# Performance work log

Hardware: AMD Instinct MI355X
Metric: run time of the kernel (lower is better)

## Reference

```python
import math
import jax, jax.numpy as jnp
import numpy as np

B, T, D, H = 2, 2048, 768, 12
DH = D // H
EPS = 1e-5


def setup_inputs() -> dict:
    key = jax.random.key(0)
    ks = jax.random.split(key, 8)
    s = 0.02
    x = jax.random.normal(ks[0], (B, T, D), dtype=jnp.float32)
    lengths = jax.random.randint(ks[1], (B,), T // 2, T + 1)
    lengths = lengths.at[0].set(T)  # ensure max(lengths)==T (static shape)
    return {
        'x': x,
        'lengths': lengths,
        'w_qkv': jax.random.normal(ks[2], (D, 3 * D), dtype=jnp.float32) * s,
        'b_qkv': jnp.zeros((3 * D,), jnp.float32),
        'w_proj': jax.random.normal(ks[3], (D, D), dtype=jnp.float32) * s,
        'b_proj': jnp.zeros((D,), jnp.float32),
        'ln1_g': jnp.ones((D,), jnp.float32),
        'ln1_b': jnp.zeros((D,), jnp.float32),
        'w_fc': jax.random.normal(ks[4], (D, 4 * D), dtype=jnp.float32) * s,
        'b_fc': jnp.zeros((4 * D,), jnp.float32),
        'w_out': jax.random.normal(ks[5], (4 * D, D), dtype=jnp.float32) * s,
        'b_out': jnp.zeros((D,), jnp.float32),
        'ln2_g': jnp.ones((D,), jnp.float32),
        'ln2_b': jnp.zeros((D,), jnp.float32),
    }


def _gelu(x):
    c = math.sqrt(2.0 / math.pi)
    return 0.5 * x * (1.0 + jnp.tanh(c * (x + 0.044715 * x * x * x)))


def _layernorm(x, g, b):
    mu = jnp.mean(x, axis=-1, keepdims=True)
    var = jnp.mean(jnp.square(x - mu), axis=-1, keepdims=True)
    return (x - mu) * jax.lax.rsqrt(var + EPS) * g + b


def _block(x, lengths, w_qkv, b_qkv, w_proj, b_proj, ln1_g, ln1_b,
           w_fc, b_fc, w_out, b_out, ln2_g, ln2_b):
    dt = x.dtype
    # [B, T] validity mask from ragged lengths
    pos = jnp.arange(T)
    mask = (pos[None, :] < lengths[:, None]).astype(dt)

    # --- SeqMultiHeadAttention (scale=False) ---
    qkv = x @ w_qkv + b_qkv  # [B, T, 3D]
    q, k, v = jnp.split(qkv, 3, axis=-1)

    def split_heads(t):  # [B,T,D] -> [B,H,T,DH]
        return t.reshape(B, T, H, DH).transpose(0, 2, 1, 3)

    q, k, v = split_heads(q), split_heads(k), split_heads(v)
    w = jnp.einsum('bhqd,bhkd->bhqk', q, k)  # [B,H,T,T]
    amask = (mask[:, None, :, None] * mask[:, None, None, :])  # [B,1,T,T]
    w = w * amask + (-1e9) * (1.0 - amask)
    w = jax.nn.softmax(w, axis=-1) * amask
    a = jnp.einsum('bhqk,bhkd->bhqd', w, v)  # [B,H,T,DH]
    a = a.transpose(0, 2, 1, 3).reshape(B, T, D)
    a = a @ w_proj + b_proj

    # --- SeqLayerNorm 1: pack/unpack == per-position LN, padding zeroed ---
    n = _layernorm(x + a, ln1_g, ln1_b) * mask[..., None]

    # --- MLP (gelu) ---
    m = _gelu(n @ w_fc + b_fc) @ w_out + b_out

    # --- SeqLayerNorm 2 ---
    h = _layernorm(n + m, ln2_g, ln2_b) * mask[..., None]
    return h


def reference(x, lengths, w_qkv, b_qkv, w_proj, b_proj, ln1_g, ln1_b,
              w_fc, b_fc, w_out, b_out, ln2_g, ln2_b):
    return _block(x, lengths, w_qkv, b_qkv, w_proj, b_proj, ln1_g, ln1_b,
                  w_fc, b_fc, w_out, b_out, ln2_g, ln2_b)
```

## Files before the change

kernel.cpp:

```cpp
#include <hip/hip_runtime.h>
#include <hip/hip_bf16.h>
#include <math.h>

constexpr int Bc  = 2;
constexpr int Tc  = 2048;
constexpr int Dc  = 768;
constexpr int Hc  = 12;
constexpr int DHc = 64;
constexpr int M_ROWS = Bc * Tc;
constexpr int D3  = 3 * Dc;
constexpr int D4  = 4 * Dc;

typedef __attribute__((ext_vector_type(8))) short short8;
typedef __attribute__((ext_vector_type(4))) float f32x4;

__device__ __forceinline__ unsigned short f2bf(float v) {
    union { __hip_bfloat16 b; unsigned short u; } cv;
    cv.b = __float2bfloat16(v);
    return cv.u;
}
__device__ __forceinline__ float bf2f(unsigned short u) {
    union { __hip_bfloat16 b; unsigned short u; } cv;
    cv.u = u;
    return __bfloat162float(cv.b);
}
__device__ __forceinline__ void bsplit(float v, unsigned short& h, unsigned short& l) {
    h = f2bf(v);
    l = f2bf(v - bf2f(h));
}

__device__ __forceinline__ float gelu_f(float x) {
    const float c = 0.79788456080286535588f;
    return 0.5f * x * (1.0f + tanhf(c * (x + 0.044715f * x * x * x)));
}

__device__ __forceinline__ void glds16(const unsigned short* g, unsigned short* l) {
    __builtin_amdgcn_global_load_lds(
        (const __attribute__((address_space(1))) void*)g,
        (__attribute__((address_space(3))) void*)l, 16, 0, 0);
}

__device__ __forceinline__ void tcast8(
    const float* __restrict__ w, int ldw,
    unsigned short* __restrict__ th, int K, int N, int idx)
{
    const int n  = idx % N;
    const int k0 = (idx / N) * 8;
    unsigned short hv[8];
#pragma unroll
    for (int j = 0; j < 8; ++j)
        hv[j] = f2bf(w[(size_t)(k0 + j) * ldw + n]);
    const size_t o = (size_t)n * K + k0;
    *(ushort4*)(th + o)     = make_ushort4(hv[0], hv[1], hv[2], hv[3]);
    *(ushort4*)(th + o + 4) = make_ushort4(hv[4], hv[5], hv[6], hv[7]);
}

__global__ __launch_bounds__(256) void prepare_kernel(
    const float* __restrict__ x,
    const float* __restrict__ w_qkv, const float* __restrict__ w_proj,
    const float* __restrict__ w_fc,  const float* __restrict__ w_out,
    unsigned short* __restrict__ xh,
    unsigned short* __restrict__ wqkvT, unsigned short* __restrict__ wprojT,
    unsigned short* __restrict__ wfcT,  unsigned short* __restrict__ woutT)
{
    int id = blockIdx.x * 256 + threadIdx.x;
    if (id < 786432) {
        const float4 v = *(const float4*)(x + (size_t)id * 4);
        *(ushort4*)(xh + (size_t)id * 4) =
            make_ushort4(f2bf(v.x), f2bf(v.y), f2bf(v.z), f2bf(v.w));
        return;
    }
    id -= 786432;
    if (id < 221184) { tcast8(w_qkv, D3, wqkvT, Dc, D3, id); return; }
    id -= 221184;
    if (id < 73728)  { tcast8(w_proj, Dc, wprojT, Dc, Dc, id); return; }
    id -= 73728;
    if (id < 294912) { tcast8(w_fc, D4, wfcT, Dc, D4, id); return; }
    id -= 294912;
    tcast8(w_out, Dc, woutT, D4, Dc, id);
}

template <int TM, int MODE>
__global__ __launch_bounds__(256) void gemm_bf16(
    const unsigned short* __restrict__ A,
    const unsigned short* __restrict__ B,
    const float* __restrict__ bias,
    float* __restrict__ C, unsigned short* __restrict__ Cb,
    int M, int N, int K)
{
    constexpr int MT = TM / 32;
    __shared__ unsigned short Ash[TM * 32];
    __shared__ unsigned short Bsh[128 * 32];

    const int tid  = threadIdx.x;
    const int n0   = blockIdx.x * 128;
    const int m0   = blockIdx.y * TM;
    const int wave = tid >> 6;
    const int lane = tid & 63;
    const int wm   = (wave >> 1) * (TM / 2);
    const int wn   = (wave & 1) * 64;
    const int lrow = lane & 15;
    const int quad = lane >> 4;

    f32x4 acc[MT][4];
    const f32x4 zero = {0.f, 0.f, 0.f, 0.f};
#pragma unroll
    for (int i = 0; i < MT; ++i)
#pragma unroll
        for (int j = 0; j < 4; ++j) acc[i][j] = zero;

    const int srow = lane >> 2;
    const int sch  = (lane & 3) * 8;

    for (int ks = 0; ks < K; ks += 32) {
        __syncthreads();
#pragma unroll
        for (int j = 0; j < TM / 64; ++j) {
            const int rbase = wave * (TM / 4) + j * 16;
            const size_t g = (size_t)(m0 + rbase + srow) * K + ks + sch;
            glds16(A + g, &Ash[rbase * 32]);
        }
#pragma unroll
        for (int j = 0; j < 2; ++j) {
            const int rbase = wave * 32 + j * 16;
            const size_t g = (size_t)(n0 + rbase + srow) * K + ks + sch;
            glds16(B + g, &Bsh[rbase * 32]);
        }
        __syncthreads();

        short8 fa[MT], fb[4];
#pragma unroll
        for (int t = 0; t < MT; ++t)
            fa[t] = *(const short8*)&Ash[(wm + t * 16 + lrow) * 32 + quad * 8];
#pragma unroll
        for (int t = 0; t < 4; ++t)
            fb[t] = *(const short8*)&Bsh[(wn + t * 16 + lrow) * 32 + quad * 8];
#pragma unroll
        for (int mt = 0; mt < MT; ++mt)
#pragma unroll
            for (int nt = 0; nt < 4; ++nt)
                acc[mt][nt] = __builtin_amdgcn_mfma_f32_16x16x32_bf16(fa[mt], fb[nt], acc[mt][nt], 0, 0, 0);
    }

#pragma unroll
    for (int mt = 0; mt < MT; ++mt) {
        const int rowb = m0 + wm + mt * 16 + quad * 4;
#pragma unroll
        for (int nt = 0; nt < 4; ++nt) {
            const int col = n0 + wn + nt * 16 + lrow;
            const float bv = bias[col];
#pragma unroll
            for (int r = 0; r < 4; ++r) {
                const size_t ci = (size_t)(rowb + r) * N + col;
                if (MODE == 0) {
                    C[ci] = acc[mt][nt][r] + bv;
                } else if (MODE == 1) {
                    Cb[ci] = f2bf(gelu_f(acc[mt][nt][r] + bv));
                } else {
                    Cb[ci] = f2bf(acc[mt][nt][r] + bv);
                }
            }
        }
    }
}

constexpr int KS  = 72;
constexpr int PS2 = 72;

__global__ __launch_bounds__(256) void flash_attn_bf16(
    const unsigned short* __restrict__ qkv,
    const int* __restrict__ lengths,
    unsigned short* __restrict__ oh)
{
    __shared__ unsigned short Kh[64 * KS];
    __shared__ unsigned short Vt[64 * KS];
    __shared__ unsigned short PfU[64 * PS2];

    const int tid  = threadIdx.x;
    const int wave = tid >> 6;
    const int lane = tid & 63;
    const int m    = lane & 15;
    const int quad = lane >> 4;

    const int nqt = Tc / 64;
    const int qt  = blockIdx.x % nqt;
    const int bh  = blockIdx.x / nqt;
    const int hh  = bh % Hc;
    const int b   = bh / Hc;
    const int len = lengths[b];
    const int q0  = qt * 64;
    const size_t rs = (size_t)D3;
    const unsigned short* base = qkv + (size_t)b * Tc * rs;
    const int qcol = hh * DHc;
    const int kcol = Dc + hh * DHc;
    const int vcol = 2 * Dc + hh * DHc;

    short8 Qf[2];
#pragma unroll
    for (int ch = 0; ch < 2; ++ch) {
        const size_t ga = (size_t)(q0 + wave * 16 + m) * rs + qcol + ch * 32 + quad * 8;
        Qf[ch] = *(const short8*)&base[ga];
    }

    f32x4 Oacc[4];
    const f32x4 zero = {0.f, 0.f, 0.f, 0.f};
#pragma unroll
    for (int nt = 0; nt < 4; ++nt) Oacc[nt] = zero;
    float lrow[4] = {0.f, 0.f, 0.f, 0.f};

    const int kr0 = tid >> 3,          kc0 = (tid & 7) * 8;
    const int kr1 = (tid + 256) >> 3,  kc1 = ((tid + 256) & 7) * 8;
    const int pk  = (tid >> 4) * 4;
    const int pd  = (tid & 15) * 4;

    short8  pK0, pK1;
    ushort4 pV0, pV1, pV2, pV3;
    {
        pK0 = *(const short8*)&base[(size_t)kr0 * rs + kcol + kc0];
        pK1 = *(const short8*)&base[(size_t)kr1 * rs + kcol + kc1];
        pV0 = *(const ushort4*)&base[(size_t)(pk + 0) * rs + vcol + pd];
        pV1 = *(const ushort4*)&base[(size_t)(pk + 1) * rs + vcol + pd];
        pV2 = *(const ushort4*)&base[(size_t)(pk + 2) * rs + vcol + pd];
        pV3 = *(const ushort4*)&base[(size_t)(pk + 3) * rs + vcol + pd];
    }

    for (int kt = 0; kt < Tc / 64; ++kt) {
        const int kbase = kt * 64;
        __syncthreads();

        *(short8*)&Kh[kr0 * KS + kc0] = pK0;
        *(short8*)&Kh[kr1 * KS + kc1] = pK1;
        *(ushort4*)&Vt[(pd + 0) * KS + pk] = make_ushort4(pV0.x, pV1.x, pV2.x, pV3.x);
        *(ushort4*)&Vt[(pd + 1) * KS + pk] = make_ushort4(pV0.y, pV1.y, pV2.y, pV3.y);
        *(ushort4*)&Vt[(pd + 2) * KS + pk] = make_ushort4(pV0.z, pV1.z, pV2.z, pV3.z);
        *(ushort4*)&Vt[(pd + 3) * KS + pk] = make_ushort4(pV0.w, pV1.w, pV2.w, pV3.w);
        __syncthreads();

        if (kt + 1 < Tc / 64) {
            const int nb = kbase + 64;
            pK0 = *(const short8*)&base[(size_t)(nb + kr0) * rs + kcol + kc0];
            pK1 = *(const short8*)&base[(size_t)(nb + kr1) * rs + kcol + kc1];
            pV0 = *(const ushort4*)&base[(size_t)(nb + pk + 0) * rs + vcol + pd];
            pV1 = *(const ushort4*)&base[(size_t)(nb + pk + 1) * rs + vcol + pd];
            pV2 = *(const ushort4*)&base[(size_t)(nb + pk + 2) * rs + vcol + pd];
            pV3 = *(const ushort4*)&base[(size_t)(nb + pk + 3) * rs + vcol + pd];
        }

        f32x4 S4[4];
#pragma unroll
        for (int nt = 0; nt < 4; ++nt) S4[nt] = zero;
#pragma unroll
        for (int ch = 0; ch < 2; ++ch)
#pragma unroll
            for (int nt = 0; nt < 4; ++nt) {
                const short8 k8 = *(const short8*)&Kh[(nt * 16 + m) * KS + ch * 32 + quad * 8];
                S4[nt] = __builtin_amdgcn_mfma_f32_16x16x32_bf16(Qf[ch], k8, S4[nt], 0, 0, 0);
            }

        if (kbase + 64 > len) {
#pragma unroll
            for (int nt = 0; nt < 4; ++nt)
                if (kbase + nt * 16 + m >= len) {
#pragma unroll
                    for (int r = 0; r < 4; ++r) S4[nt][r] = -1e30f;
                }
        }

#pragma unroll
        for (int nt = 0; nt < 4; ++nt)
#pragma unroll
            for (int r = 0; r < 4; ++r) {
                const float p = __expf(S4[nt][r]);
                lrow[r] += p;
                PfU[(wave * 16 + quad * 4 + r) * PS2 + nt * 16 + m] = f2bf(p);
            }

#pragma unroll
        for (int ch = 0; ch < 2; ++ch) {
            const short8 P8 = *(const short8*)&PfU[(wave * 16 + m) * PS2 + ch * 32 + quad * 8];
#pragma unroll
            for (int nt = 0; nt < 4; ++nt) {
                const short8 v8 = *(const short8*)&Vt[(nt * 16 + m) * KS + ch * 32 + quad * 8];
                Oacc[nt] = __builtin_amdgcn_mfma_f32_16x16x32_bf16(P8, v8, Oacc[nt], 0, 0, 0);
            }
        }
    }

#pragma unroll
    for (int r = 0; r < 4; ++r) {
#pragma unroll
        for (int sh = 8; sh >= 1; sh >>= 1)
            lrow[r] += __shfl_xor(lrow[r], sh);
    }

#pragma unroll
    for (int r = 0; r < 4; ++r) {
        const int qrow = q0 + wave * 16 + quad * 4 + r;
        const size_t ob = (size_t)(b * Tc + qrow) * Dc + hh * DHc + m;
        if (qrow < len) {
            const float inv = 1.0f / lrow[r];
#pragma unroll
            for (int nt = 0; nt < 4; ++nt)
                oh[ob + nt * 16] = f2bf(Oacc[nt][r] * inv);
        } else {
#pragma unroll
            for (int nt = 0; nt < 4; ++nt)
                oh[ob + nt * 16] = 0;
        }
    }
}

__global__ __launch_bounds__(256) void ln_split_kernel(
    const float* __restrict__ X, const float* __restrict__ Y,
    const float* __restrict__ g, const float* __restrict__ beta,
    const int* __restrict__ lengths,
    unsigned short* __restrict__ outh, unsigned short* __restrict__ outl)
{
    __shared__ float red[4];
    const int row = blockIdx.x;
    const int b = row / Tc, t = row % Tc;
    const int len = lengths[b];
    const size_t basei = (size_t)row * Dc;
    const int tid = threadIdx.x;

    if (t >= len) {
        for (int j = tid; j < Dc; j += 256) { outh[basei + j] = 0; outl[basei + j] = 0; }
        return;
    }

    float v[3];
    float s = 0.f;
#pragma unroll
    for (int j = 0; j < 3; ++j) {
        int idx = tid + j * 256;
        v[j] = X[basei + idx] + Y[basei + idx];
        s += v[j];
    }
    const int lane = tid % 64, wid = tid / 64;
#pragma unroll
    for (int sh = 32; sh >= 1; sh >>= 1) s += __shfl_xor(s, sh);
    if (lane == 0) red[wid] = s;
    __syncthreads();
    s = red[0] + red[1] + red[2] + red[3];
    const float mu = s * (1.0f / Dc);

    float vs = 0.f;
#pragma unroll
    for (int j = 0; j < 3; ++j) { float dv = v[j] - mu; vs += dv * dv; }
    __syncthreads();
#pragma unroll
    for (int sh = 32; sh >= 1; sh >>= 1) vs += __shfl_xor(vs, sh);
    if (lane == 0) red[wid] = vs;
    __syncthreads();
    vs = red[0] + red[1] + red[2] + red[3];
    const float rstd = rsqrtf(vs * (1.0f / Dc) + 1e-5f);

#pragma unroll
    for (int j = 0; j < 3; ++j) {
        int idx = tid + j * 256;
        const float ov = (v[j] - mu) * rstd * g[idx] + beta[idx];
        unsigned short hh, ll;
        bsplit(ov, hh, ll);
        outh[basei + idx] = hh;
        outl[basei + idx] = ll;
    }
}

__global__ __launch_bounds__(256) void ln2_kernel(
    const unsigned short* __restrict__ Xh, const unsigned short* __restrict__ Xl,
    const float* Y,
    const float* __restrict__ g, const float* __restrict__ beta,
    const int* __restrict__ lengths, float* out)
{
    __shared__ float red[4];
    const int row = blockIdx.x;
    const int b = row / Tc, t = row % Tc;
    const int len = lengths[b];
    const size_t basei = (size_t)row * Dc;
    const int tid = threadIdx.x;

    if (t >= len) {
        for (int j = tid; j < Dc; j += 256) out[basei + j] = 0.f;
        return;
    }

    float v[3];
    float s = 0.f;
#pragma unroll
    for (int j = 0; j < 3; ++j) {
        int idx = tid + j * 256;
        v[j] = bf2f(Xh[basei + idx]) + bf2f(Xl[basei + idx]) + Y[basei + idx];
        s += v[j];
    }
    const int lane = tid % 64, wid = tid / 64;
#pragma unroll
    for (int sh = 32; sh >= 1; sh >>= 1) s += __shfl_xor(s, sh);
    if (lane == 0) red[wid] = s;
    __syncthreads();
    s = red[0] + red[1] + red[2] + red[3];
    const float mu = s * (1.0f / Dc);

    float vs = 0.f;
#pragma unroll
    for (int j = 0; j < 3; ++j) { float dv = v[j] - mu; vs += dv * dv; }
    __syncthreads();
#pragma unroll
    for (int sh = 32; sh >= 1; sh >>= 1) vs += __shfl_xor(vs, sh);
    if (lane == 0) red[wid] = vs;
    __syncthreads();
    vs = red[0] + red[1] + red[2] + red[3];
    const float rstd = rsqrtf(vs * (1.0f / Dc) + 1e-5f);

#pragma unroll
    for (int j = 0; j < 3; ++j) {
        int idx = tid + j * 256;
        out[basei + idx] = (v[j] - mu) * rstd * g[idx] + beta[idx];
    }
}

extern "C" void kernel_launch(void* const* d_in, const int* in_sizes, int n_in,
                              void* d_out, int out_size, void* d_ws, size_t ws_size,
                              hipStream_t stream)
{
    const float* x      = (const float*)d_in[0];
    const int*   lens   = (const int*)  d_in[1];
    const float* w_qkv  = (const float*)d_in[2];
    const float* b_qkv  = (const float*)d_in[3];
    const float* w_proj = (const float*)d_in[4];
    const float* b_proj = (const float*)d_in[5];
    const float* ln1_g  = (const float*)d_in[6];
    const float* ln1_b  = (const float*)d_in[7];
    const float* w_fc   = (const float*)d_in[8];
    const float* b_fc   = (const float*)d_in[9];
    const float* w_out  = (const float*)d_in[10];
    const float* b_out  = (const float*)d_in[11];
    const float* ln2_g  = (const float*)d_in[12];
    const float* ln2_b  = (const float*)d_in[13];

    if (ws_size < 51904512) return;

    char* ws = (char*)d_ws;
    unsigned short* qkvh  = (unsigned short*)(ws + 0);
    unsigned short* xh    = (unsigned short*)(ws + 18874368);
    unsigned short* ah    = xh;
    float*          projo = (float*)(ws + 0);
    unsigned short* fH    = (unsigned short*)(ws + 0);
    unsigned short* nh    = (unsigned short*)(ws + 25165824);
    unsigned short* nl    = (unsigned short*)(ws + 31457280);
    unsigned short* wqkvT = (unsigned short*)(ws + 37748736);
    unsigned short* wprojT= (unsigned short*)(ws + 41287680);
    unsigned short* wfcT  = (unsigned short*)(ws + 42467328);
    unsigned short* woutT = (unsigned short*)(ws + 47185920);
    float*          mbuf  = (float*)d_out;

    const dim3 blk(256);

    prepare_kernel<<<dim3(6528), blk, 0, stream>>>(
        x, w_qkv, w_proj, w_fc, w_out, xh, wqkvT, wprojT, wfcT, woutT);

    gemm_bf16<128, 3><<<dim3(D3 / 128, M_ROWS / 128), blk, 0, stream>>>(
        xh, wqkvT, b_qkv, nullptr, qkvh, M_ROWS, D3, Dc);

    flash_attn_bf16<<<dim3(Bc * Hc * (Tc / 64)), blk, 0, stream>>>(qkvh, lens, ah);

    gemm_bf16<64, 0><<<dim3(Dc / 128, M_ROWS / 64), blk, 0, stream>>>(
        ah, wprojT, b_proj, projo, nullptr, M_ROWS, Dc, Dc);

    ln_split_kernel<<<dim3(M_ROWS), blk, 0, stream>>>(x, projo, ln1_g, ln1_b, lens, nh, nl);

    gemm_bf16<128, 1><<<dim3(D4 / 128, M_ROWS / 128), blk, 0, stream>>>(
        nh, wfcT, b_fc, nullptr, fH, M_ROWS, D4, Dc);

    gemm_bf16<64, 0><<<dim3(Dc / 128, M_ROWS / 64), blk, 0, stream>>>(
        fH, woutT, b_out, mbuf, nullptr, M_ROWS, Dc, D4);

    ln2_kernel<<<dim3(M_ROWS), blk, 0, stream>>>(nh, nl, mbuf, ln2_g, ln2_b, lens,
                                                 (float*)d_out);
}
```

Baseline: 347.5 us.

## Deepen GEMM K-step with swizzled LDS, skip padded attention tiles, use exp2

The GEMM now stages 64-wide K slices per iteration and reads shared memory through an XOR swizzle. This halves the number of barriers per K and is meant to reduce bank conflicts, at the cost of doubling LDS use per block. The attention kernel now writes zeros and exits early for query tiles past the sequence length, and stops the key loop at the valid length. This skips work that only produces masked-out values. Q is prescaled by log2(e) so exp2 can replace expf, and V^T is stored with a swizzle to cut LDS conflicts; the prescale adds an extra bf16 rounding of Q.

```diff
diff --git a/kernel.cpp b/kernel.cpp
--- a/kernel.cpp
+++ b/kernel.cpp
@@ -89,8 +89,8 @@
     int M, int N, int K)
 {
     constexpr int MT = TM / 32;
-    __shared__ unsigned short Ash[TM * 32];
-    __shared__ unsigned short Bsh[128 * 32];
+    __shared__ unsigned short Ash[TM * 64];
+    __shared__ unsigned short Bsh[128 * 64];
 
     const int tid  = threadIdx.x;
     const int n0   = blockIdx.x * 128;
@@ -101,6 +101,7 @@
     const int wn   = (wave & 1) * 64;
     const int lrow = lane & 15;
     const int quad = lane >> 4;
+    const int swz  = lrow & 7;
 
     f32x4 acc[MT][4];
     const f32x4 zero = {0.f, 0.f, 0.f, 0.f};
@@ -109,37 +110,43 @@
 #pragma unroll
         for (int j = 0; j < 4; ++j) acc[i][j] = zero;
 
-    const int srow = lane >> 2;
-    const int sch  = (lane & 3) * 8;
-
-    for (int ks = 0; ks < K; ks += 32) {
+    const int l8r  = lane >> 3;
+    const int csel = ((lane & 7) ^ l8r) * 8;
+
+    for (int ks = 0; ks < K; ks += 64) {
         __syncthreads();
 #pragma unroll
-        for (int j = 0; j < TM / 64; ++j) {
-            const int rbase = wave * (TM / 4) + j * 16;
-            const size_t g = (size_t)(m0 + rbase + srow) * K + ks + sch;
-            glds16(A + g, &Ash[rbase * 32]);
-        }
-#pragma unroll
-        for (int j = 0; j < 2; ++j) {
-            const int rbase = wave * 32 + j * 16;
-            const size_t g = (size_t)(n0 + rbase + srow) * K + ks + sch;
-            glds16(B + g, &Bsh[rbase * 32]);
+        for (int j = 0; j < TM / 32; ++j) {
+            const int rbase = wave * (TM / 4) + j * 8;
+            const size_t g = (size_t)(m0 + rbase + l8r) * K + ks + csel;
+            glds16(A + g, &Ash[rbase * 64]);
+        }
+#pragma unroll
+        for (int j = 0; j < 4; ++j) {
+            const int rbase = wave * 32 + j * 8;
+            const size_t g = (size_t)(n0 + rbase + l8r) * K + ks + csel;
+            glds16(B + g, &Bsh[rbase * 64]);
         }
         __syncthreads();
 
-        short8 fa[MT], fb[4];
-#pragma unroll
-        for (int t = 0; t < MT; ++t)
-            fa[t] = *(const short8*)&Ash[(wm + t * 16 + lrow) * 32 + quad * 8];
-#pragma unroll
-        for (int t = 0; t < 4; ++t)
-            fb[t] = *(const short8*)&Bsh[(wn + t * 16 + lrow) * 32 + quad * 8];
-#pragma unroll
-        for (int mt = 0; mt < MT; ++mt)
-#pragma unroll
-            for (int nt = 0; nt < 4; ++nt)
-                acc[mt][nt] = __builtin_amdgcn_mfma_f32_16x16x32_bf16(fa[mt], fb[nt], acc[mt][nt], 0, 0, 0);
+#pragma unroll
+        for (int kk = 0; kk < 2; ++kk) {
+            short8 fa[MT], fb[4];
+            const int cl = kk * 4 + quad;
+            const int pc = (cl ^ swz) * 8;
+#pragma unroll
+            for (int t = 0; t < MT; ++t)
+                fa[t] = *(const short8*)&Ash[(wm + t * 16 + lrow) * 64 + pc];
+#pragma unroll
+            for (int t = 0; t < 4; ++t)
+                fb[t] = *(const short8*)&Bsh[(wn + t * 16 + lrow) * 64 + pc];
+#pragma unroll
+            for (int mt = 0; mt < MT; ++mt)
+#pragma unroll
+                for (int nt = 0; nt < 4; ++nt)
+                    acc[mt][nt] = __builtin_amdgcn_mfma_f32_16x16x32_bf16(
+                        fa[mt], fb[nt], acc[mt][nt], 0, 0, 0);
+        }
     }
 
 #pragma unroll
@@ -195,11 +202,29 @@
     const int kcol = Dc + hh * DHc;
     const int vcol = 2 * Dc + hh * DHc;
 
+    if (q0 >= len) {
+#pragma unroll
+        for (int r = 0; r < 4; ++r) {
+            const int qrow = q0 + wave * 16 + quad * 4 + r;
+            const size_t ob = (size_t)(b * Tc + qrow) * Dc + hh * DHc + m;
+#pragma unroll
+            for (int nt = 0; nt < 4; ++nt) oh[ob + nt * 16] = 0;
+        }
+        return;
+    }
+
+    const int ktEnd = (min(len, Tc) + 63) >> 6;
+
     short8 Qf[2];
 #pragma unroll
     for (int ch = 0; ch < 2; ++ch) {
         const size_t ga = (size_t)(q0 + wave * 16 + m) * rs + qcol + ch * 32 + quad * 8;
-        Qf[ch] = *(const short8*)&base[ga];
+        const short8 q8 = *(const short8*)&base[ga];
+        short8 qs;
+#pragma unroll
+        for (int j = 0; j < 8; ++j)
+            qs[j] = (short)f2bf(bf2f((unsigned short)q8[j]) * 1.44269504088896f);
+        Qf[ch] = qs;
     }
 
     f32x4 Oacc[4];
@@ -212,6 +237,7 @@
     const int kr1 = (tid + 256) >> 3,  kc1 = ((tid + 256) & 7) * 8;
     const int pk  = (tid >> 4) * 4;
     const int pd  = (tid & 15) * 4;
+    const int vswz = ((pk >> 3) ^ ((pd >> 2) & 7)) * 8 + (pk & 7);
 
     short8  pK0, pK1;
     ushort4 pV0, pV1, pV2, pV3;
@@ -224,19 +250,19 @@
         pV3 = *(const ushort4*)&base[(size_t)(pk + 3) * rs + vcol + pd];
     }
 
-    for (int kt = 0; kt < Tc / 64; ++kt) {
+    for (int kt = 0; kt < ktEnd; ++kt) {
         const int kbase = kt * 64;
         __syncthreads();
 
         *(short8*)&Kh[kr0 * KS + kc0] = pK0;
         *(short8*)&Kh[kr1 * KS + kc1] = pK1;
-        *(ushort4*)&Vt[(pd + 0) * KS + pk] = make_ushort4(pV0.x, pV1.x, pV2.x, pV3.x);
-        *(ushort4*)&Vt[(pd + 1) * KS + pk] = make_ushort4(pV0.y, pV1.y, pV2.y, pV3.y);
-        *(ushort4*)&Vt[(pd + 2) * KS + pk] = make_ushort4(pV0.z, pV1.z, pV2.z, pV3.z);
-        *(ushort4*)&Vt[(pd + 3) * KS + pk] = make_ushort4(pV0.w, pV1.w, pV2.w, pV3.w);
+        *(ushort4*)&Vt[(pd + 0) * KS + vswz] = make_ushort4(pV0.x, pV1.x, pV2.x, pV3.x);
+        *(ushort4*)&Vt[(pd + 1) * KS + vswz] = make_ushort4(pV0.y, pV1.y, pV2.y, pV3.y);
+        *(ushort4*)&Vt[(pd + 2) * KS + vswz] = make_ushort4(pV0.z, pV1.z, pV2.z, pV3.z);
+        *(ushort4*)&Vt[(pd + 3) * KS + vswz] = make_ushort4(pV0.w, pV1.w, pV2.w, pV3.w);
         __syncthreads();
 
-        if (kt + 1 < Tc / 64) {
+        if (kt + 1 < ktEnd) {
             const int nb = kbase + 64;
             pK0 = *(const short8*)&base[(size_t)(nb + kr0) * rs + kcol + kc0];
             pK1 = *(const short8*)&base[(size_t)(nb + kr1) * rs + kcol + kc1];
@@ -270,7 +296,7 @@
         for (int nt = 0; nt < 4; ++nt)
 #pragma unroll
             for (int r = 0; r < 4; ++r) {
-                const float p = __expf(S4[nt][r]);
+                const float p = __builtin_amdgcn_exp2f(S4[nt][r]);
                 lrow[r] += p;
                 PfU[(wave * 16 + quad * 4 + r) * PS2 + nt * 16 + m] = f2bf(p);
             }
@@ -280,7 +306,8 @@
             const short8 P8 = *(const short8*)&PfU[(wave * 16 + m) * PS2 + ch * 32 + quad * 8];
 #pragma unroll
             for (int nt = 0; nt < 4; ++nt) {
-                const short8 v8 = *(const short8*)&Vt[(nt * 16 + m) * KS + ch * 32 + quad * 8];
+                const int pchunk = ((ch * 4 + quad) ^ ((nt * 4 + (m >> 2)) & 7)) * 8;
+                const short8 v8 = *(const short8*)&Vt[(nt * 16 + m) * KS + pchunk];
                 Oacc[nt] = __builtin_amdgcn_mfma_f32_16x16x32_bf16(P8, v8, Oacc[nt], 0, 0, 0);
             }
         }
```

New measurement: 306.9 us. -11.7%, faster.
